# Performance work log

Measured on AMD Instinct MI355X. Metric: run time of the kernel, lower is better.

## Reference

```python
import jax, jax.numpy as jnp
import numpy as np

EPS = 1e-5


def gated_graph_conv(x, edge_index, W, w_ih, w_hh, b_ih, b_hh):
    # W: [num_layers, C, C]; PyG pads input features up to out_channels C.
    N = x.shape[0]
    C = W.shape[1]
    if x.shape[1] < C:
        x = jnp.pad(x, ((0, 0), (0, C - x.shape[1])))
    src, dst = edge_index[0], edge_index[1]
    for i in range(W.shape[0]):
        m = x @ W[i]                                   # [N, C]
        agg = jax.ops.segment_sum(m[src], dst, num_segments=N)  # scatter-add aggr
        # GRUCell(agg, x)
        gi = agg @ w_ih.T + b_ih                       # [N, 3C]
        gh = x @ w_hh.T + b_hh
        ir, iz, in_ = jnp.split(gi, 3, axis=-1)
        hr, hz, hn = jnp.split(gh, 3, axis=-1)
        r = jax.nn.sigmoid(ir + hr)
        z = jax.nn.sigmoid(iz + hz)
        n = jnp.tanh(in_ + r * hn)
        x = (1.0 - z) * n + z * x
    return x


def batch_norm_eval(x, gamma, beta, mean, var):
    return (x - mean) * jax.lax.rsqrt(var + EPS) * gamma + beta


def _ggc_params(key, C):
    ks = jax.random.split(key, 5)
    s = 1.0 / np.sqrt(C)
    return (jax.random.uniform(ks[0], (4, C, C), minval=-s, maxval=s),
            jax.random.uniform(ks[1], (3 * C, C), minval=-s, maxval=s),
            jax.random.uniform(ks[2], (3 * C, C), minval=-s, maxval=s),
            jax.random.uniform(ks[3], (3 * C,), minval=-s, maxval=s),
            jax.random.uniform(ks[4], (3 * C,), minval=-s, maxval=s))


def _bn_params(key, C):
    ks = jax.random.split(key, 4)
    return (jax.random.normal(ks[0], (C,)) * 0.1 + 1.0,
            jax.random.normal(ks[1], (C,)) * 0.1,
            jax.random.normal(ks[2], (C,)) * 0.1,
            jax.random.uniform(ks[3], (C,), minval=0.5, maxval=1.5))


def setup_inputs() -> dict:
    key = jax.random.key(0)
    N, E, NF, NG, NA = 50000, 800000, 32, 256, 10
    ks = jax.random.split(key, 12)
    x = jax.random.normal(ks[0], (N, NF), dtype=jnp.float32)
    edge_index = jax.random.randint(ks[1], (2, E), 0, N, dtype=jnp.int64)
    batch = jnp.sort(jax.random.randint(ks[2], (N,), 0, NG, dtype=jnp.int64))
    c1 = _ggc_params(ks[3], NF)
    c2 = _ggc_params(ks[4], 64)
    c3 = _ggc_params(ks[5], 128)
    bn1 = _bn_params(ks[6], NF)
    bn2 = _bn_params(ks[7], 64)
    s1 = 1.0 / np.sqrt(128)
    fc1_W = jax.random.uniform(ks[8], (256, 128), minval=-s1, maxval=s1)
    fc1_b = jax.random.uniform(ks[9], (256,), minval=-s1, maxval=s1)
    s2 = 1.0 / np.sqrt(256)
    fc2_W = jax.random.uniform(ks[10], (NA, 256), minval=-s2, maxval=s2)
    fc2_b = jax.random.uniform(ks[11], (NA,), minval=-s2, maxval=s2)
    d = {"x": x, "edge_index": edge_index, "batch": batch,
         "fc1_W": fc1_W, "fc1_b": fc1_b, "fc2_W": fc2_W, "fc2_b": fc2_b}
    for name, p in (("conv1", c1), ("conv2", c2), ("conv3", c3)):
        d[name + "_W"], d[name + "_wih"], d[name + "_whh"], d[name + "_bih"], d[name + "_bhh"] = p
    for name, p in (("bn1", bn1), ("bn2", bn2)):
        d[name + "_gamma"], d[name + "_beta"], d[name + "_mean"], d[name + "_var"] = p
    return d


def reference(x, edge_index, batch,
              conv1_W, conv1_wih, conv1_whh, conv1_bih, conv1_bhh,
              conv2_W, conv2_wih, conv2_whh, conv2_bih, conv2_bhh,
              conv3_W, conv3_wih, conv3_whh, conv3_bih, conv3_bhh,
              bn1_gamma, bn1_beta, bn1_mean, bn1_var,
              bn2_gamma, bn2_beta, bn2_mean, bn2_var,
              fc1_W, fc1_b, fc2_W, fc2_b):
    NUM_GRAPHS = 256
    h = jax.nn.elu(gated_graph_conv(x, edge_index, conv1_W, conv1_wih, conv1_whh, conv1_bih, conv1_bhh))
    h = batch_norm_eval(h, bn1_gamma, bn1_beta, bn1_mean, bn1_var)
    h = jax.nn.elu(gated_graph_conv(h, edge_index, conv2_W, conv2_wih, conv2_whh, conv2_bih, conv2_bhh))
    h = batch_norm_eval(h, bn2_gamma, bn2_beta, bn2_mean, bn2_var)
    h = jax.nn.elu(gated_graph_conv(h, edge_index, conv3_W, conv3_wih, conv3_whh, conv3_bih, conv3_bhh))
    g = jax.ops.segment_sum(h, batch, num_segments=NUM_GRAPHS)  # global_add_pool
    g = jax.nn.elu(g @ fc1_W.T + fc1_b)
    # dropout is identity in eval mode
    return jax.nn.log_softmax(g @ fc2_W.T + fc2_b, axis=-1)
```

## Files before the change

### kernel.cpp

```cpp
#include <hip/hip_runtime.h>
#include <math.h>


#define EPS_BN 1e-5f

typedef short short8 __attribute__((ext_vector_type(8)));
typedef unsigned short u16x8 __attribute__((ext_vector_type(8)));
typedef float f32x4 __attribute__((ext_vector_type(4)));

__device__ __forceinline__ float elu_f(float v) {
    return v > 0.f ? v : expm1f(v);
}
__device__ __forceinline__ float sigmoid_f(float v) {
    return 1.f / (1.f + __expf(-v));
}
__device__ __forceinline__ float tanh_f(float v) {
    float e = __expf(2.f * v);
    return 1.f - 2.f / (e + 1.f);
}
__device__ __forceinline__ unsigned short f2bf(float f) {
    unsigned u = __float_as_uint(f);
    unsigned r = (u + 0x7FFF + ((u >> 16) & 1)) >> 16;
    return (unsigned short)r;
}
__device__ __forceinline__ float bf2f(unsigned short b) {
    return __uint_as_float(((unsigned)b) << 16);
}
__device__ __forceinline__ void put_hl(unsigned short* __restrict__ hi,
                                       unsigned short* __restrict__ lo,
                                       size_t idx, float v) {
    unsigned short h = f2bf(v);
    hi[idx] = h;
    lo[idx] = f2bf(v - bf2f(h));
}


__global__ __launch_bounds__(256) void hist_kernel(
    const int* __restrict__ ei, int* __restrict__ deg, int E) {
    int e = blockIdx.x * 256 + threadIdx.x;
    if (e < E) atomicAdd(&deg[ei[E + e]], 1);
}

__global__ __launch_bounds__(256) void scan1_kernel(
    const int* __restrict__ deg, int* __restrict__ out,
    int* __restrict__ blockSums, int N) {
    __shared__ int sdata[256];
    int b = blockIdx.x, t = threadIdx.x;
    int base = b * 1024 + t * 4;
    int v[4], s = 0;
#pragma unroll
    for (int i = 0; i < 4; ++i) {
        v[i] = (base + i < N) ? deg[base + i] : 0;
        s += v[i];
    }
    sdata[t] = s;
    __syncthreads();
    for (int off = 1; off < 256; off <<= 1) {
        int x = (t >= off) ? sdata[t - off] : 0;
        __syncthreads();
        sdata[t] += x;
        __syncthreads();
    }
    int run = sdata[t] - s;
#pragma unroll
    for (int i = 0; i < 4; ++i) {
        if (base + i < N) out[base + i] = run;
        run += v[i];
    }
    if (t == 255) blockSums[b] = sdata[255];
}

__global__ void scan2_kernel(int* blockSums, int nb) {
    if (threadIdx.x == 0 && blockIdx.x == 0) {
        int run = 0;
        for (int i = 0; i < nb; ++i) {
            int v = blockSums[i];
            blockSums[i] = run;
            run += v;
        }
    }
}

__global__ __launch_bounds__(256) void scan3_kernel(
    const int* __restrict__ out, const int* __restrict__ blockSums,
    int* __restrict__ rowstart, int* __restrict__ writeptr, int N, int E) {
    int i = blockIdx.x * 256 + threadIdx.x;
    if (i < N) {
        int v = out[i] + blockSums[i >> 10];
        rowstart[i] = v;
        writeptr[i] = v;
    }
    if (i == 0) rowstart[N] = E;
}

__global__ __launch_bounds__(256) void fill_kernel(
    const int* __restrict__ ei, int* __restrict__ writeptr,
    int* __restrict__ csr_src, int E) {
    int e = blockIdx.x * 256 + threadIdx.x;
    if (e < E) {
        int d = ei[E + e];
        int p = atomicAdd(&writeptr[d], 1);
        csr_src[p] = ei[e];
    }
}


template <int C>
__global__ __launch_bounds__(256) void wc_kernel(
    const float* __restrict__ W, const float* __restrict__ wih,
    float* __restrict__ Wc) {
    int idx = blockIdx.x * 256 + threadIdx.x;
    if (idx >= 4 * C * 3 * C) return;
    int l = idx / (C * 3 * C);
    int r = idx % (C * 3 * C);
    int k = r / (3 * C);
    int row = r % (3 * C);
    const float* wrow = W + ((size_t)l * C + k) * C;
    const float* irow = wih + (size_t)row * C;
    float acc = 0.f;
#pragma unroll 4
    for (int t = 0; t < C; ++t) acc += wrow[t] * irow[t];
    Wc[idx] = acc;
}


template <int C>
__global__ __launch_bounds__(256) void swizzle_b2_kernel(
    const float* __restrict__ Wc, const float* __restrict__ whh,
    unsigned short* __restrict__ BsHi, unsigned short* __restrict__ BsLo) {
    constexpr int CT = C / 16;
    int idx = blockIdx.x * 256 + threadIdx.x;
    if (idx >= 4 * 6 * C * C) return;
    int l = idx / (6 * C * C);
    int r0 = idx % (6 * C * C);
    int j = r0 & 7;
    int lane = (r0 >> 3) & 63;
    int rest = r0 >> 9;
    int tslot = rest % (3 * CT);
    int ks = rest / (3 * CT);
    int k = ks * 32 + (lane >> 4) * 8 + j;
    int g = tslot / CT;
    int lt = tslot % CT;
    int c = lt * 16 + (lane & 15);
    int row = g * C + c;
    float v = (k < C) ? Wc[((size_t)l * C + k) * 3 * C + row]
                      : whh[(size_t)row * C + (k - C)];
    unsigned short h = f2bf(v);
    BsHi[idx] = h;
    BsLo[idx] = f2bf(v - bf2f(h));
}


template <int C>
__global__ __launch_bounds__(256) void gather_kernel(
    const unsigned short* __restrict__ Xhi,
    const int* __restrict__ rowstart, const int* __restrict__ csr_src,
    unsigned short* __restrict__ Shi, int N) {
    constexpr int LPG = C / 8;
    constexpr int GPB = 256 / LPG;
    int lane = threadIdx.x % LPG;
    int grp = threadIdx.x / LPG;
    int d = blockIdx.x * GPB + grp;
    if (d >= N) return;
    int p = rowstart[d];
    int p1 = rowstart[d + 1];
    float a[8];
#pragma unroll
    for (int j = 0; j < 8; ++j) a[j] = 0.f;
    int off = lane * 8;
    for (; p + 3 < p1; p += 4) {
        int s0 = csr_src[p];
        int s1 = csr_src[p + 1];
        int s2 = csr_src[p + 2];
        int s3 = csr_src[p + 3];
        u16x8 h0 = *(const u16x8*)(Xhi + (size_t)s0 * C + off);
        u16x8 h1 = *(const u16x8*)(Xhi + (size_t)s1 * C + off);
        u16x8 h2 = *(const u16x8*)(Xhi + (size_t)s2 * C + off);
        u16x8 h3 = *(const u16x8*)(Xhi + (size_t)s3 * C + off);
#pragma unroll
        for (int j = 0; j < 8; ++j) {
            a[j] += (bf2f(h0[j]) + bf2f(h1[j])) + (bf2f(h2[j]) + bf2f(h3[j]));
        }
    }
    for (; p < p1; ++p) {
        int s0 = csr_src[p];
        u16x8 h0 = *(const u16x8*)(Xhi + (size_t)s0 * C + off);
#pragma unroll
        for (int j = 0; j < 8; ++j) a[j] += bf2f(h0[j]);
    }
    size_t base = (size_t)d * C + off;
#pragma unroll
    for (int j = 0; j < 8; ++j) Shi[base + j] = f2bf(a[j]);
}


template <int C, int MINW>
__global__ __launch_bounds__(256, MINW) void gru_mfma_kernel(
    const unsigned short* __restrict__ HinHi, const unsigned short* __restrict__ HinLo,
    unsigned short* __restrict__ HoutHi, unsigned short* __restrict__ HoutLo,
    const unsigned short* __restrict__ Shi,
    const unsigned short* __restrict__ BsHi, const unsigned short* __restrict__ BsLo,
    const float* __restrict__ biasI, const float* __restrict__ biasH, int N) {
    constexpr int CT = C / 16;
    constexpr int KS = C / 16;
    constexpr int CTW = CT / 4;
    int wave = threadIdx.x >> 6;
    int lane = threadIdx.x & 63;
    int quad = lane >> 4;
    int l16 = lane & 15;
    int node0 = blockIdx.x * 64;
    int arow[4];
#pragma unroll
    for (int t = 0; t < 4; ++t) {
        int r = node0 + t * 16 + l16;
        arow[t] = r < N ? r : N - 1;
    }
    f32x4 accR[CTW][4], accZ[CTW][4], accN[CTW][4], accH[CTW][4];
#pragma unroll
    for (int ct = 0; ct < CTW; ++ct)
#pragma unroll
        for (int t = 0; t < 4; ++t) {
            accR[ct][t] = (f32x4){0.f, 0.f, 0.f, 0.f};
            accZ[ct][t] = (f32x4){0.f, 0.f, 0.f, 0.f};
            accN[ct][t] = (f32x4){0.f, 0.f, 0.f, 0.f};
            accH[ct][t] = (f32x4){0.f, 0.f, 0.f, 0.f};
        }
    const short8* bhi = (const short8*)BsHi;
    const short8* blo = (const short8*)BsLo;

    for (int ks = 0; ks < KS / 2; ++ks) {
        int k0 = ks * 32 + quad * 8;
        short8 ahi[4];
#pragma unroll
        for (int t = 0; t < 4; ++t)
            ahi[t] = *(const short8*)(Shi + (size_t)arow[t] * C + k0);
#pragma unroll
        for (int ct = 0; ct < CTW; ++ct) {
            int ts = ks * 3 * CT + wave * CTW + ct;
            short8 bhf = bhi[(size_t)ts * 64 + lane];
            short8 blf = blo[(size_t)ts * 64 + lane];
#pragma unroll
            for (int t = 0; t < 4; ++t) {
                accR[ct][t] = __builtin_amdgcn_mfma_f32_16x16x32_bf16(ahi[t], bhf, accR[ct][t], 0, 0, 0);
                accR[ct][t] = __builtin_amdgcn_mfma_f32_16x16x32_bf16(ahi[t], blf, accR[ct][t], 0, 0, 0);
            }
            bhf = bhi[(size_t)(ts + CT) * 64 + lane];
            blf = blo[(size_t)(ts + CT) * 64 + lane];
#pragma unroll
            for (int t = 0; t < 4; ++t) {
                accZ[ct][t] = __builtin_amdgcn_mfma_f32_16x16x32_bf16(ahi[t], bhf, accZ[ct][t], 0, 0, 0);
                accZ[ct][t] = __builtin_amdgcn_mfma_f32_16x16x32_bf16(ahi[t], blf, accZ[ct][t], 0, 0, 0);
            }
            bhf = bhi[(size_t)(ts + 2 * CT) * 64 + lane];
            blf = blo[(size_t)(ts + 2 * CT) * 64 + lane];
#pragma unroll
            for (int t = 0; t < 4; ++t) {
                accN[ct][t] = __builtin_amdgcn_mfma_f32_16x16x32_bf16(ahi[t], bhf, accN[ct][t], 0, 0, 0);
                accN[ct][t] = __builtin_amdgcn_mfma_f32_16x16x32_bf16(ahi[t], blf, accN[ct][t], 0, 0, 0);
            }
        }
    }
    for (int ks = KS / 2; ks < KS; ++ks) {
        int k0 = ks * 32 + quad * 8 - C;
        short8 ahi[4], alo[4];
#pragma unroll
        for (int t = 0; t < 4; ++t) {
            ahi[t] = *(const short8*)(HinHi + (size_t)arow[t] * C + k0);
            alo[t] = *(const short8*)(HinLo + (size_t)arow[t] * C + k0);
        }
#pragma unroll
        for (int ct = 0; ct < CTW; ++ct) {
            int ts = ks * 3 * CT + wave * CTW + ct;
            short8 bhf = bhi[(size_t)ts * 64 + lane];
            short8 blf = blo[(size_t)ts * 64 + lane];
#pragma unroll
            for (int t = 0; t < 4; ++t) {
                accR[ct][t] = __builtin_amdgcn_mfma_f32_16x16x32_bf16(ahi[t], bhf, accR[ct][t], 0, 0, 0);
                accR[ct][t] = __builtin_amdgcn_mfma_f32_16x16x32_bf16(alo[t], bhf, accR[ct][t], 0, 0, 0);
                accR[ct][t] = __builtin_amdgcn_mfma_f32_16x16x32_bf16(ahi[t], blf, accR[ct][t], 0, 0, 0);
            }
            bhf = bhi[(size_t)(ts + CT) * 64 + lane];
            blf = blo[(size_t)(ts + CT) * 64 + lane];
#pragma unroll
            for (int t = 0; t < 4; ++t) {
                accZ[ct][t] = __builtin_amdgcn_mfma_f32_16x16x32_bf16(ahi[t], bhf, accZ[ct][t], 0, 0, 0);
                accZ[ct][t] = __builtin_amdgcn_mfma_f32_16x16x32_bf16(alo[t], bhf, accZ[ct][t], 0, 0, 0);
                accZ[ct][t] = __builtin_amdgcn_mfma_f32_16x16x32_bf16(ahi[t], blf, accZ[ct][t], 0, 0, 0);
            }
            bhf = bhi[(size_t)(ts + 2 * CT) * 64 + lane];
            blf = blo[(size_t)(ts + 2 * CT) * 64 + lane];
#pragma unroll
            for (int t = 0; t < 4; ++t) {
                accH[ct][t] = __builtin_amdgcn_mfma_f32_16x16x32_bf16(ahi[t], bhf, accH[ct][t], 0, 0, 0);
                accH[ct][t] = __builtin_amdgcn_mfma_f32_16x16x32_bf16(alo[t], bhf, accH[ct][t], 0, 0, 0);
                accH[ct][t] = __builtin_amdgcn_mfma_f32_16x16x32_bf16(ahi[t], blf, accH[ct][t], 0, 0, 0);
            }
        }
    }

#pragma unroll
    for (int ct = 0; ct < CTW; ++ct) {
        int c = (wave * CTW + ct) * 16 + l16;
        float bir = biasI[c], biz = biasI[C + c], bin = biasI[2 * C + c];
        float bhr = biasH[c], bhz = biasH[C + c], bhn = biasH[2 * C + c];
#pragma unroll
        for (int t = 0; t < 4; ++t) {
#pragma unroll
            for (int r = 0; r < 4; ++r) {
                int node = node0 + t * 16 + quad * 4 + r;
                if (node < N) {
                    size_t gi = (size_t)node * C + c;
                    float xo = bf2f(HinHi[gi]) + bf2f(HinLo[gi]);
                    float rv = sigmoid_f(accR[ct][t][r] + bir + bhr);
                    float zv = sigmoid_f(accZ[ct][t][r] + biz + bhz);
                    float nv = tanh_f(accN[ct][t][r] + bin + rv * (accH[ct][t][r] + bhn));
                    put_hl(HoutHi, HoutLo, gi, (1.f - zv) * nv + zv * xo);
                }
            }
        }
    }
}

__global__ __launch_bounds__(256, 4) void gru32_kernel(
    const unsigned short* __restrict__ HinHi, const unsigned short* __restrict__ HinLo,
    unsigned short* __restrict__ HoutHi, unsigned short* __restrict__ HoutLo,
    const unsigned short* __restrict__ Shi,
    const unsigned short* __restrict__ BsHi, const unsigned short* __restrict__ BsLo,
    const float* __restrict__ biasI, const float* __restrict__ biasH, int N) {
    constexpr int C = 32;
    constexpr int CT = 2;
    int wave = threadIdx.x >> 6;
    int lane = threadIdx.x & 63;
    int quad = lane >> 4;
    int l16 = lane & 15;
    int node0 = blockIdx.x * 64 + wave * 16;
    int ar = node0 + l16;
    if (ar >= N) ar = N - 1;
    f32x4 accR[CT], accZ[CT], accN[CT], accH[CT];
#pragma unroll
    for (int t = 0; t < CT; ++t) {
        accR[t] = (f32x4){0.f, 0.f, 0.f, 0.f};
        accZ[t] = (f32x4){0.f, 0.f, 0.f, 0.f};
        accN[t] = (f32x4){0.f, 0.f, 0.f, 0.f};
        accH[t] = (f32x4){0.f, 0.f, 0.f, 0.f};
    }
    const short8* bhi = (const short8*)BsHi;
    const short8* blo = (const short8*)BsLo;
    int k0 = quad * 8;
    {
        short8 ahi = *(const short8*)(Shi + (size_t)ar * C + k0);
#pragma unroll
        for (int g = 0; g < 3; ++g) {
            f32x4* acc = g == 0 ? accR : (g == 1 ? accZ : accN);
#pragma unroll
            for (int t = 0; t < CT; ++t) {
                int ts = g * CT + t;
                short8 bhf = bhi[(size_t)ts * 64 + lane];
                short8 blf = blo[(size_t)ts * 64 + lane];
                acc[t] = __builtin_amdgcn_mfma_f32_16x16x32_bf16(ahi, bhf, acc[t], 0, 0, 0);
                acc[t] = __builtin_amdgcn_mfma_f32_16x16x32_bf16(ahi, blf, acc[t], 0, 0, 0);
            }
        }
    }
    {
        short8 ahi = *(const short8*)(HinHi + (size_t)ar * C + k0);
        short8 alo = *(const short8*)(HinLo + (size_t)ar * C + k0);
#pragma unroll
        for (int g = 0; g < 3; ++g) {
            f32x4* acc = g == 0 ? accR : (g == 1 ? accZ : accH);
#pragma unroll
            for (int t = 0; t < CT; ++t) {
                int ts = 3 * CT + g * CT + t;
                short8 bhf = bhi[(size_t)ts * 64 + lane];
                short8 blf = blo[(size_t)ts * 64 + lane];
                acc[t] = __builtin_amdgcn_mfma_f32_16x16x32_bf16(ahi, bhf, acc[t], 0, 0, 0);
                acc[t] = __builtin_amdgcn_mfma_f32_16x16x32_bf16(alo, bhf, acc[t], 0, 0, 0);
                acc[t] = __builtin_amdgcn_mfma_f32_16x16x32_bf16(ahi, blf, acc[t], 0, 0, 0);
            }
        }
    }
#pragma unroll
    for (int t = 0; t < CT; ++t) {
        int c = t * 16 + l16;
        float bir = biasI[c], biz = biasI[C + c], bin = biasI[2 * C + c];
        float bhr = biasH[c], bhz = biasH[C + c], bhn = biasH[2 * C + c];
#pragma unroll
        for (int r = 0; r < 4; ++r) {
            int node = node0 + quad * 4 + r;
            if (node < N) {
                size_t gi = (size_t)node * C + c;
                float xo = bf2f(HinHi[gi]) + bf2f(HinLo[gi]);
                float rv = sigmoid_f(accR[t][r] + bir + bhr);
                float zv = sigmoid_f(accZ[t][r] + biz + bhz);
                float nv = tanh_f(accN[t][r] + bin + rv * (accH[t][r] + bhn));
                put_hl(HoutHi, HoutLo, gi, (1.f - zv) * nv + zv * xo);
            }
        }
    }
}


__global__ __launch_bounds__(256) void init_x_kernel(
    const float* __restrict__ x, unsigned short* __restrict__ Hhi,
    unsigned short* __restrict__ Hlo, int total) {
    int t = blockIdx.x * 256 + threadIdx.x;
    if (t < total) put_hl(Hhi, Hlo, t, x[t]);
}

template <int Cin, int Cout>
__global__ __launch_bounds__(256) void elu_bn_pad_kernel(
    const unsigned short* __restrict__ Shi, const unsigned short* __restrict__ Slo,
    unsigned short* __restrict__ Dhi, unsigned short* __restrict__ Dlo,
    const float* __restrict__ gamma, const float* __restrict__ beta,
    const float* __restrict__ mean, const float* __restrict__ var, int N) {
    long t = (long)blockIdx.x * 256 + threadIdx.x;
    long total = (long)N * Cout;
    if (t >= total) return;
    int n = (int)(t / Cout);
    int c = (int)(t & (Cout - 1));
    float v = 0.f;
    if (c < Cin) {
        size_t si = (size_t)n * Cin + c;
        float x = bf2f(Shi[si]) + bf2f(Slo[si]);
        x = elu_f(x);
        v = (x - mean[c]) * rsqrtf(var[c] + EPS_BN) * gamma[c] + beta[c];
    }
    put_hl(Dhi, Dlo, t, v);
}

__global__ __launch_bounds__(256) void pool_elu_kernel(
    const unsigned short* __restrict__ Hhi, const unsigned short* __restrict__ Hlo,
    const int* __restrict__ batch, float* __restrict__ G, int N) {
    long t = (long)blockIdx.x * 256 + threadIdx.x;
    if (t >= (long)N * 128) return;
    int n = (int)(t >> 7);
    int c = (int)(t & 127);
    float v = elu_f(bf2f(Hhi[t]) + bf2f(Hlo[t]));
    atomicAdd(&G[batch[n] * 128 + c], v);
}

__global__ __launch_bounds__(256) void fc1_kernel(
    const float* __restrict__ G, const float* __restrict__ W,
    const float* __restrict__ b, float* __restrict__ G2) {
    __shared__ float row[128];
    int g = blockIdx.x;
    int j = threadIdx.x;
    if (j < 128) row[j] = G[g * 128 + j];
    __syncthreads();
    float acc = b[j];
    for (int k = 0; k < 128; ++k) acc += row[k] * W[j * 128 + k];
    G2[g * 256 + j] = elu_f(acc);
}

__global__ __launch_bounds__(64) void fc2_logsoftmax_kernel(
    const float* __restrict__ G2, const float* __restrict__ W,
    const float* __restrict__ b, float* __restrict__ out) {
    __shared__ float row[256];
    __shared__ float logits[10];
    __shared__ float red[2];
    int g = blockIdx.x;
    int tid = threadIdx.x;
    for (int i = tid; i < 256; i += 64) row[i] = G2[g * 256 + i];
    __syncthreads();
    if (tid < 10) {
        float acc = b[tid];
        for (int k = 0; k < 256; ++k) acc += row[k] * W[tid * 256 + k];
        logits[tid] = acc;
    }
    __syncthreads();
    if (tid == 0) {
        float m = -1e30f;
        for (int a = 0; a < 10; ++a) m = fmaxf(m, logits[a]);
        float s = 0.f;
        for (int a = 0; a < 10; ++a) s += expf(logits[a] - m);
        red[0] = m;
        red[1] = logf(s);
    }
    __syncthreads();
    if (tid < 10) out[g * 10 + tid] = logits[tid] - red[0] - red[1];
}


template <int C>
static void run_conv(unsigned short* Ahi, unsigned short* Alo,
                     unsigned short* Bhi, unsigned short* Blo,
                     unsigned short* Shi,
                     float* Wc, unsigned short* BsHi, unsigned short* BsLo,
                     const float* W, const float* wih, const float* whh,
                     const float* bih, const float* bhh,
                     const int* rowstart, const int* csr_src,
                     int N, int E, hipStream_t stream) {
    wc_kernel<C><<<(4 * C * 3 * C + 255) / 256, 256, 0, stream>>>(W, wih, Wc);
    swizzle_b2_kernel<C><<<(4 * 6 * C * C + 255) / 256, 256, 0, stream>>>(Wc, whh, BsHi, BsLo);
    int nb = (N + 63) / 64;
    constexpr int GPB = 2048 / C;
    int gblocks = (N + GPB - 1) / GPB;
    unsigned short *inHi = Ahi, *inLo = Alo, *outHi = Bhi, *outLo = Blo;
    for (int it = 0; it < 4; ++it) {
        gather_kernel<C><<<gblocks, 256, 0, stream>>>(
            inHi, rowstart, csr_src, Shi, N);
        const unsigned short* bs_h = BsHi + (size_t)it * 6 * C * C;
        const unsigned short* bs_l = BsLo + (size_t)it * 6 * C * C;
        if constexpr (C == 32)
            gru32_kernel<<<nb, 256, 0, stream>>>(
                inHi, inLo, outHi, outLo, Shi, bs_h, bs_l, bih, bhh, N);
        else
            gru_mfma_kernel<C, (C == 128 ? 2 : 3)><<<nb, 256, 0, stream>>>(
                inHi, inLo, outHi, outLo, Shi, bs_h, bs_l, bih, bhh, N);
        unsigned short* tp;
        tp = inHi; inHi = outHi; outHi = tp;
        tp = inLo; inLo = outLo; outLo = tp;
    }
}

extern "C" void kernel_launch(void* const* d_in, const int* in_sizes, int n_in,
                              void* d_out, int out_size, void* d_ws, size_t ws_size,
                              hipStream_t stream) {
    const float* x = (const float*)d_in[0];
    const int* ei = (const int*)d_in[1];
    const int* batch = (const int*)d_in[2];
    const float* fc1W = (const float*)d_in[3];
    const float* fc1b = (const float*)d_in[4];
    const float* fc2W = (const float*)d_in[5];
    const float* fc2b = (const float*)d_in[6];
    const float* c1W = (const float*)d_in[7];
    const float* c1wih = (const float*)d_in[8];
    const float* c1whh = (const float*)d_in[9];
    const float* c1bih = (const float*)d_in[10];
    const float* c1bhh = (const float*)d_in[11];
    const float* c2W = (const float*)d_in[12];
    const float* c2wih = (const float*)d_in[13];
    const float* c2whh = (const float*)d_in[14];
    const float* c2bih = (const float*)d_in[15];
    const float* c2bhh = (const float*)d_in[16];
    const float* c3W = (const float*)d_in[17];
    const float* c3wih = (const float*)d_in[18];
    const float* c3whh = (const float*)d_in[19];
    const float* c3bih = (const float*)d_in[20];
    const float* c3bhh = (const float*)d_in[21];
    const float* bn1g = (const float*)d_in[22];
    const float* bn1b = (const float*)d_in[23];
    const float* bn1m = (const float*)d_in[24];
    const float* bn1v = (const float*)d_in[25];
    const float* bn2g = (const float*)d_in[26];
    const float* bn2b = (const float*)d_in[27];
    const float* bn2m = (const float*)d_in[28];
    const float* bn2v = (const float*)d_in[29];

    int N = in_sizes[0] / 32;
    int E = in_sizes[1] / 2;

    const size_t NB = (size_t)N * 128;
    unsigned short* PAhi = (unsigned short*)d_ws;
    unsigned short* PAlo = PAhi + NB;
    unsigned short* PBhi = PAlo + NB;
    unsigned short* PBlo = PBhi + NB;
    unsigned short* Shi = PBlo + NB;
    unsigned short* Slo = Shi + NB;
    unsigned short* BsHi = Slo + NB;
    unsigned short* BsLo = BsHi + 393216;
    float* Wc = (float*)(BsLo + 393216);
    float* G = Wc + 196608;
    float* G2 = G + 32768;
    int* deg = (int*)(G2 + 65536);
    int* scanout = deg + N;
    int* rowstart = scanout + N;
    int* writeptr = rowstart + N + 1;
    int* blockSums = writeptr + N;
    int* csr_src = blockSums + 64;

    hipMemsetAsync(deg, 0, (size_t)N * sizeof(int), stream);
    int eblocks = (E + 255) / 256;
    hist_kernel<<<eblocks, 256, 0, stream>>>(ei, deg, E);
    int nscan = (N + 1023) / 1024;
    scan1_kernel<<<nscan, 256, 0, stream>>>(deg, scanout, blockSums, N);
    scan2_kernel<<<1, 64, 0, stream>>>(blockSums, nscan);
    scan3_kernel<<<(N + 255) / 256, 256, 0, stream>>>(scanout, blockSums, rowstart, writeptr, N, E);
    fill_kernel<<<eblocks, 256, 0, stream>>>(ei, writeptr, csr_src, E);

    init_x_kernel<<<(N * 32 + 255) / 256, 256, 0, stream>>>(x, PAhi, PAlo, N * 32);

    run_conv<32>(PAhi, PAlo, PBhi, PBlo, Shi, Wc, BsHi, BsLo,
                 c1W, c1wih, c1whh, c1bih, c1bhh, rowstart, csr_src, N, E, stream);
    elu_bn_pad_kernel<32, 64><<<(int)(((long)N * 64 + 255) / 256), 256, 0, stream>>>(
        PAhi, PAlo, PBhi, PBlo, bn1g, bn1b, bn1m, bn1v, N);

    run_conv<64>(PBhi, PBlo, PAhi, PAlo, Shi, Wc, BsHi, BsLo,
                 c2W, c2wih, c2whh, c2bih, c2bhh, rowstart, csr_src, N, E, stream);
    elu_bn_pad_kernel<64, 128><<<(int)(((long)N * 128 + 255) / 256), 256, 0, stream>>>(
        PBhi, PBlo, PAhi, PAlo, bn2g, bn2b, bn2m, bn2v, N);

    run_conv<128>(PAhi, PAlo, PBhi, PBlo, Shi, Wc, BsHi, BsLo,
                  c3W, c3wih, c3whh, c3bih, c3bhh, rowstart, csr_src, N, E, stream);

    hipMemsetAsync(G, 0, 256 * 128 * sizeof(float), stream);
    pool_elu_kernel<<<(int)(((long)N * 128 + 255) / 256), 256, 0, stream>>>(
        PAhi, PAlo, batch, G, N);

    fc1_kernel<<<256, 256, 0, stream>>>(G, fc1W, fc1b, G2);
    fc2_logsoftmax_kernel<<<256, 64, 0, stream>>>(G2, fc2W, fc2b, (float*)d_out);
}
```

Before: 940.9 us.

## Fuse CSR neighbor gather into GRU MFMA kernels via swizzled LDS tile

Removes the separate gather kernel and has each 64-node GRU block first aggregate its own nodes' neighbor features into a swizzled shared-memory tile, then read its MFMA A operands from LDS. This drops the global write and reread of the aggregated buffer and twelve kernel launches. In exchange the gather phase no longer overlaps with MFMA work across separate launches, LDS use per block grows, and gather parallelism is tied to the GRU grid and occupancy limits.

After: 984.9 us. 4.7% more time.

```diff
diff --git a/kernel.cpp b/kernel.cpp
--- a/kernel.cpp
+++ b/kernel.cpp
@@ -32,6 +32,14 @@
     unsigned short h = f2bf(v);
     hi[idx] = h;
     lo[idx] = f2bf(v - bf2f(h));
+}
+
+template <int C>
+__device__ __forceinline__ int s_swz(int row, int byteoff) {
+    if constexpr (C == 32)
+        return byteoff ^ (((row >> 1) & 3) << 4);
+    else
+        return byteoff ^ ((row & 7) << 4);
 }
 
 
@@ -151,64 +159,71 @@
 }
 
 
-template <int C>
-__global__ __launch_bounds__(256) void gather_kernel(
-    const unsigned short* __restrict__ Xhi,
-    const int* __restrict__ rowstart, const int* __restrict__ csr_src,
-    unsigned short* __restrict__ Shi, int N) {
-    constexpr int LPG = C / 8;
-    constexpr int GPB = 256 / LPG;
-    int lane = threadIdx.x % LPG;
-    int grp = threadIdx.x / LPG;
-    int d = blockIdx.x * GPB + grp;
-    if (d >= N) return;
-    int p = rowstart[d];
-    int p1 = rowstart[d + 1];
-    float a[8];
-#pragma unroll
-    for (int j = 0; j < 8; ++j) a[j] = 0.f;
-    int off = lane * 8;
-    for (; p + 3 < p1; p += 4) {
-        int s0 = csr_src[p];
-        int s1 = csr_src[p + 1];
-        int s2 = csr_src[p + 2];
-        int s3 = csr_src[p + 3];
-        u16x8 h0 = *(const u16x8*)(Xhi + (size_t)s0 * C + off);
-        u16x8 h1 = *(const u16x8*)(Xhi + (size_t)s1 * C + off);
-        u16x8 h2 = *(const u16x8*)(Xhi + (size_t)s2 * C + off);
-        u16x8 h3 = *(const u16x8*)(Xhi + (size_t)s3 * C + off);
-#pragma unroll
-        for (int j = 0; j < 8; ++j) {
-            a[j] += (bf2f(h0[j]) + bf2f(h1[j])) + (bf2f(h2[j]) + bf2f(h3[j]));
-        }
-    }
-    for (; p < p1; ++p) {
-        int s0 = csr_src[p];
-        u16x8 h0 = *(const u16x8*)(Xhi + (size_t)s0 * C + off);
-#pragma unroll
-        for (int j = 0; j < 8; ++j) a[j] += bf2f(h0[j]);
-    }
-    size_t base = (size_t)d * C + off;
-#pragma unroll
-    for (int j = 0; j < 8; ++j) Shi[base + j] = f2bf(a[j]);
-}
-
-
 template <int C, int MINW>
-__global__ __launch_bounds__(256, MINW) void gru_mfma_kernel(
+__global__ __launch_bounds__(256, MINW) void gru_fused_kernel(
     const unsigned short* __restrict__ HinHi, const unsigned short* __restrict__ HinLo,
     unsigned short* __restrict__ HoutHi, unsigned short* __restrict__ HoutLo,
-    const unsigned short* __restrict__ Shi,
+    const int* __restrict__ rowstart, const int* __restrict__ csr_src,
     const unsigned short* __restrict__ BsHi, const unsigned short* __restrict__ BsLo,
     const float* __restrict__ biasI, const float* __restrict__ biasH, int N) {
     constexpr int CT = C / 16;
     constexpr int KS = C / 16;
     constexpr int CTW = CT / 4;
+    constexpr int LPG = C / 8;
+    constexpr int GPB = 256 / LPG;
+    constexpr int PASSES = 64 / GPB;
+    __shared__ unsigned short Slds[64 * C];
+
+    int node0 = blockIdx.x * 64;
+
+    {
+        int glane = threadIdx.x % LPG;
+        int grp = threadIdx.x / LPG;
+        int off = glane * 8;
+#pragma unroll
+        for (int pass = 0; pass < PASSES; ++pass) {
+            int dl = pass * GPB + grp;
+            int d = node0 + dl;
+            float a[8];
+#pragma unroll
+            for (int j = 0; j < 8; ++j) a[j] = 0.f;
+            if (d < N) {
+                int p = rowstart[d];
+                int p1 = rowstart[d + 1];
+                for (; p + 3 < p1; p += 4) {
+                    int s0 = csr_src[p];
+                    int s1 = csr_src[p + 1];
+                    int s2 = csr_src[p + 2];
+                    int s3 = csr_src[p + 3];
+                    u16x8 h0 = *(const u16x8*)(HinHi + (size_t)s0 * C + off);
+                    u16x8 h1 = *(const u16x8*)(HinHi + (size_t)s1 * C + off);
+                    u16x8 h2 = *(const u16x8*)(HinHi + (size_t)s2 * C + off);
+                    u16x8 h3 = *(const u16x8*)(HinHi + (size_t)s3 * C + off);
+#pragma unroll
+                    for (int j = 0; j < 8; ++j) {
+                        a[j] += (bf2f(h0[j]) + bf2f(h1[j])) + (bf2f(h2[j]) + bf2f(h3[j]));
+                    }
+                }
+                for (; p < p1; ++p) {
+                    int s0 = csr_src[p];
+                    u16x8 h0 = *(const u16x8*)(HinHi + (size_t)s0 * C + off);
+#pragma unroll
+                    for (int j = 0; j < 8; ++j) a[j] += bf2f(h0[j]);
+                }
+            }
+            u16x8 hv;
+#pragma unroll
+            for (int j = 0; j < 8; ++j) hv[j] = f2bf(a[j]);
+            int bo = s_swz<C>(dl, (dl * C + off) * 2);
+            *(u16x8*)((char*)Slds + bo) = hv;
+        }
+    }
+    __syncthreads();
+
     int wave = threadIdx.x >> 6;
     int lane = threadIdx.x & 63;
     int quad = lane >> 4;
     int l16 = lane & 15;
-    int node0 = blockIdx.x * 64;
     int arow[4];
 #pragma unroll
     for (int t = 0; t < 4; ++t) {
@@ -229,11 +244,14 @@
     const short8* blo = (const short8*)BsLo;
 
     for (int ks = 0; ks < KS / 2; ++ks) {
-        int k0 = ks * 32 + quad * 8;
+        int cb = ks * 64 + quad * 16;
         short8 ahi[4];
 #pragma unroll
-        for (int t = 0; t < 4; ++t)
-            ahi[t] = *(const short8*)(Shi + (size_t)arow[t] * C + k0);
+        for (int t = 0; t < 4; ++t) {
+            int row = t * 16 + l16;
+            int bo = s_swz<C>(row, row * 2 * C + cb);
+            ahi[t] = *(const short8*)((const char*)Slds + bo);
+        }
 #pragma unroll
         for (int ct = 0; ct < CTW; ++ct) {
             int ts = ks * 3 * CT + wave * CTW + ct;
@@ -321,19 +339,62 @@
     }
 }
 
-__global__ __launch_bounds__(256, 4) void gru32_kernel(
+__global__ __launch_bounds__(256, 4) void gru32_fused_kernel(
     const unsigned short* __restrict__ HinHi, const unsigned short* __restrict__ HinLo,
     unsigned short* __restrict__ HoutHi, unsigned short* __restrict__ HoutLo,
-    const unsigned short* __restrict__ Shi,
+    const int* __restrict__ rowstart, const int* __restrict__ csr_src,
     const unsigned short* __restrict__ BsHi, const unsigned short* __restrict__ BsLo,
     const float* __restrict__ biasI, const float* __restrict__ biasH, int N) {
     constexpr int C = 32;
     constexpr int CT = 2;
+    __shared__ unsigned short Slds[64 * C];
+    int blk0 = blockIdx.x * 64;
+
+    {
+        int glane = threadIdx.x & 3;
+        int dl = threadIdx.x >> 2;
+        int d = blk0 + dl;
+        int off = glane * 8;
+        float a[8];
+#pragma unroll
+        for (int j = 0; j < 8; ++j) a[j] = 0.f;
+        if (d < N) {
+            int p = rowstart[d];
+            int p1 = rowstart[d + 1];
+            for (; p + 3 < p1; p += 4) {
+                int s0 = csr_src[p];
+                int s1 = csr_src[p + 1];
+                int s2 = csr_src[p + 2];
+                int s3 = csr_src[p + 3];
+                u16x8 h0 = *(const u16x8*)(HinHi + (size_t)s0 * C + off);
+                u16x8 h1 = *(const u16x8*)(HinHi + (size_t)s1 * C + off);
+                u16x8 h2 = *(const u16x8*)(HinHi + (size_t)s2 * C + off);
+                u16x8 h3 = *(const u16x8*)(HinHi + (size_t)s3 * C + off);
+#pragma unroll
+                for (int j = 0; j < 8; ++j) {
+                    a[j] += (bf2f(h0[j]) + bf2f(h1[j])) + (bf2f(h2[j]) + bf2f(h3[j]));
+                }
+            }
+            for (; p < p1; ++p) {
+                int s0 = csr_src[p];
+                u16x8 h0 = *(const u16x8*)(HinHi + (size_t)s0 * C + off);
+#pragma unroll
+                for (int j = 0; j < 8; ++j) a[j] += bf2f(h0[j]);
+            }
+        }
+        u16x8 hv;
+#pragma unroll
+        for (int j = 0; j < 8; ++j) hv[j] = f2bf(a[j]);
+        int bo = s_swz<C>(dl, (dl * C + off) * 2);
+        *(u16x8*)((char*)Slds + bo) = hv;
+    }
+    __syncthreads();
+
     int wave = threadIdx.x >> 6;
     int lane = threadIdx.x & 63;
     int quad = lane >> 4;
     int l16 = lane & 15;
-    int node0 = blockIdx.x * 64 + wave * 16;
+    int node0 = blk0 + wave * 16;
     int ar = node0 + l16;
     if (ar >= N) ar = N - 1;
     f32x4 accR[CT], accZ[CT], accN[CT], accH[CT];
@@ -348,7 +409,9 @@
     const short8* blo = (const short8*)BsLo;
     int k0 = quad * 8;
     {
-        short8 ahi = *(const short8*)(Shi + (size_t)ar * C + k0);
+        int row = wave * 16 + l16;
+        int bo = s_swz<C>(row, row * 2 * C + quad * 16);
+        short8 ahi = *(const short8*)((const char*)Slds + bo);
 #pragma unroll
         for (int g = 0; g < 3; ++g) {
             f32x4* acc = g == 0 ? accR : (g == 1 ? accZ : accN);
@@ -484,7 +547,6 @@
 template <int C>
 static void run_conv(unsigned short* Ahi, unsigned short* Alo,
                      unsigned short* Bhi, unsigned short* Blo,
-                     unsigned short* Shi,
                      float* Wc, unsigned short* BsHi, unsigned short* BsLo,
                      const float* W, const float* wih, const float* whh,
                      const float* bih, const float* bhh,
@@ -493,20 +555,16 @@
     wc_kernel<C><<<(4 * C * 3 * C + 255) / 256, 256, 0, stream>>>(W, wih, Wc);
     swizzle_b2_kernel<C><<<(4 * 6 * C * C + 255) / 256, 256, 0, stream>>>(Wc, whh, BsHi, BsLo);
     int nb = (N + 63) / 64;
-    constexpr int GPB = 2048 / C;
-    int gblocks = (N + GPB - 1) / GPB;
     unsigned short *inHi = Ahi, *inLo = Alo, *outHi = Bhi, *outLo = Blo;
     for (int it = 0; it < 4; ++it) {
-        gather_kernel<C><<<gblocks, 256, 0, stream>>>(
-            inHi, rowstart, csr_src, Shi, N);
         const unsigned short* bs_h = BsHi + (size_t)it * 6 * C * C;
         const unsigned short* bs_l = BsLo + (size_t)it * 6 * C * C;
         if constexpr (C == 32)
-            gru32_kernel<<<nb, 256, 0, stream>>>(
-                inHi, inLo, outHi, outLo, Shi, bs_h, bs_l, bih, bhh, N);
+            gru32_fused_kernel<<<nb, 256, 0, stream>>>(
+                inHi, inLo, outHi, outLo, rowstart, csr_src, bs_h, bs_l, bih, bhh, N);
         else
-            gru_mfma_kernel<C, (C == 128 ? 2 : 3)><<<nb, 256, 0, stream>>>(
-                inHi, inLo, outHi, outLo, Shi, bs_h, bs_l, bih, bhh, N);
+            gru_fused_kernel<C, (C == 128 ? 2 : 3)><<<nb, 256, 0, stream>>>(
+                inHi, inLo, outHi, outLo, rowstart, csr_src, bs_h, bs_l, bih, bhh, N);
         unsigned short* tp;
         tp = inHi; inHi = outHi; outHi = tp;
         tp = inLo; inLo = outLo; outLo = tp;
@@ -580,17 +638,17 @@
 
     init_x_kernel<<<(N * 32 + 255) / 256, 256, 0, stream>>>(x, PAhi, PAlo, N * 32);
 
-    run_conv<32>(PAhi, PAlo, PBhi, PBlo, Shi, Wc, BsHi, BsLo,
+    run_conv<32>(PAhi, PAlo, PBhi, PBlo, Wc, BsHi, BsLo,
                  c1W, c1wih, c1whh, c1bih, c1bhh, rowstart, csr_src, N, E, stream);
     elu_bn_pad_kernel<32, 64><<<(int)(((long)N * 64 + 255) / 256), 256, 0, stream>>>(
         PAhi, PAlo, PBhi, PBlo, bn1g, bn1b, bn1m, bn1v, N);
 
-    run_conv<64>(PBhi, PBlo, PAhi, PAlo, Shi, Wc, BsHi, BsLo,
+    run_conv<64>(PBhi, PBlo, PAhi, PAlo, Wc, BsHi, BsLo,
                  c2W, c2wih, c2whh, c2bih, c2bhh, rowstart, csr_src, N, E, stream);
     elu_bn_pad_kernel<64, 128><<<(int)(((long)N * 128 + 255) / 256), 256, 0, stream>>>(
         PBhi, PBlo, PAhi, PAlo, bn2g, bn2b, bn2m, bn2v, N);
 
-    run_conv<128>(PAhi, PAlo, PBhi, PBlo, Shi, Wc, BsHi, BsLo,
+    run_conv<128>(PAhi, PAlo, PBhi, PBlo, Wc, BsHi, BsLo,
                   c3W, c3wih, c3whh, c3bih, c3bhh, rowstart, csr_src, N, E, stream);
 
     hipMemsetAsync(G, 0, 256 * 128 * sizeof(float), stream);
```
